# Kernel tuning notes

Measured on AMD Instinct MI355X. Metric: run time of the kernel, lower is better.

## Reference

```python
import jax, jax.numpy as jnp
import numpy as np

ANCHORS = np.array([116., 90., 156., 198., 373., 326.], np.float32).reshape(1, 1, 1, 3, 2)
IGNORE_THRESH = 0.5
OBJ_SCALE = 5.0
NOOBJ_SCALE = 1.0
XYWH_SCALE = 1.0
CLASS_SCALE = 1.0
GRID_SCALE = 1.0


def setup_inputs() -> dict:
    key = jax.random.key(0)
    k1, k2, k3 = jax.random.split(key, 3)
    B, GH, GW, NET, T, C = 16, 64, 64, 1024, 100, 80
    input_image = jnp.zeros((B, NET, NET, 3), jnp.float32)  # only shape is used
    y_pred = jax.random.normal(k1, (B, GH, GW, 3 * (5 + C)), jnp.float32)
    y_true = jax.random.uniform(k2, (B, GH, GW, 3, 5 + C), jnp.float32)
    true_boxes = jax.random.uniform(k3, (B, 1, 1, 1, T, 4), jnp.float32)
    return {"input_image": input_image, "y_pred": y_pred, "y_true": y_true, "true_boxes": true_boxes}


def reference(input_image, y_pred, y_true, true_boxes):
    B, GH, GW = y_true.shape[:3]
    net_h, net_w = input_image.shape[1], input_image.shape[2]
    dtype = y_pred.dtype
    anchors = jnp.asarray(ANCHORS, dtype)  # [1,1,1,3,2]
    y_pred = y_pred.reshape(B, GH, GW, 3, -1)
    object_mask = y_true[..., 4:5]  # [B,GH,GW,3,1]
    grid_factor = jnp.array([GW, GH], dtype).reshape(1, 1, 1, 1, 2)
    net_factor = jnp.array([net_w, net_h], dtype).reshape(1, 1, 1, 1, 2)
    cx, cy = jnp.meshgrid(jnp.arange(GW, dtype=dtype), jnp.arange(GH, dtype=dtype))
    cell_grid = jnp.stack([cx, cy], -1)[None, :, :, None, :]  # [1,GH,GW,1,2]

    # adjust predictions
    pred_box_xy = cell_grid + jax.nn.sigmoid(y_pred[..., :2])
    pred_box_wh = y_pred[..., 2:4]
    pred_box_conf = jax.nn.sigmoid(y_pred[..., 4:5])
    pred_box_class = y_pred[..., 5:]

    # adjust ground truth
    true_box_xy = y_true[..., 0:2]
    true_box_wh = y_true[..., 2:4]
    true_box_class = jnp.argmax(y_true[..., 5:], axis=-1)  # [B,GH,GW,3]

    # broadcast IoU: each predicted box vs all true boxes
    true_xy = true_boxes[..., 0:2] / grid_factor  # [B,1,1,1,T,2]
    true_wh = true_boxes[..., 2:4] / net_factor
    true_half = true_wh / 2.0
    true_mins, true_maxes = true_xy - true_half, true_xy + true_half
    pred_xy = (pred_box_xy / grid_factor)[..., None, :]  # [B,GH,GW,3,1,2]
    pred_wh = (jnp.exp(pred_box_wh) * anchors / net_factor)[..., None, :]
    pred_half = pred_wh / 2.0
    pred_mins, pred_maxes = pred_xy - pred_half, pred_xy + pred_half
    inter_wh = jnp.maximum(jnp.minimum(pred_maxes, true_maxes) - jnp.maximum(pred_mins, true_mins), 0.0)
    inter_area = inter_wh[..., 0] * inter_wh[..., 1]  # [B,GH,GW,3,T]
    true_area = true_wh[..., 0] * true_wh[..., 1]
    pred_area = pred_wh[..., 0] * pred_wh[..., 1]
    iou = inter_area / (pred_area + true_area - inter_area)
    best_ious = jnp.max(iou, axis=4)
    conf_ignore_mask = (best_ious > IGNORE_THRESH).astype(dtype)[..., None]

    # post-warmup branch (batch_seen > warmup_batches)
    xywh_mask = object_mask

    wh_scale = jnp.exp(true_box_wh) * anchors / net_factor
    wh_scale = (2.0 - wh_scale[..., 0] * wh_scale[..., 1])[..., None]

    xy_delta = xywh_mask * (true_box_xy - pred_box_xy) * wh_scale * XYWH_SCALE
    wh_delta = xywh_mask * (true_box_wh - pred_box_wh) * wh_scale * XYWH_SCALE
    conf_delta = (0.0 - pred_box_conf) * NOOBJ_SCALE
    conf_delta = conf_delta + object_mask * (1.0 - pred_box_conf) * OBJ_SCALE
    conf_delta = conf_delta * (1.0 - (1.0 - object_mask) * conf_ignore_mask)
    log_p = jax.nn.log_softmax(pred_box_class, axis=-1)
    ce = -jnp.take_along_axis(log_p, true_box_class[..., None], axis=-1)  # [B,GH,GW,3,1]
    class_delta = object_mask * ce * CLASS_SCALE

    delta = jnp.concatenate([xy_delta, wh_delta, conf_delta, class_delta], axis=-1)  # [B,GH,GW,3,6]
    loss = jnp.sum(jnp.square(delta), axis=(1, 2, 3, 4))
    return loss * GRID_SCALE
```

## Files before the change

kernel.cpp:

```cpp
#include <hip/hip_runtime.h>


#define NT 100
#define CPB 12288
#define NTOT 196608
#define ROWS_PER_BLOCK 64

typedef float f4 __attribute__((ext_vector_type(4)));
typedef f4 f4a __attribute__((aligned(4)));

__device__ __forceinline__ float frcp(float x) { return __builtin_amdgcn_rcpf(x); }
__device__ __forceinline__ float fsig(float x) { return frcp(1.f + __expf(-x)); }

__global__ __launch_bounds__(256) void yolo_loss_kernel(
    const float* __restrict__ y_pred,
    const float* __restrict__ y_true,
    const float* __restrict__ true_boxes,
    float* __restrict__ out)
{
    __shared__ f4 sbox[NT];
    __shared__ float swsum[4];

    const int tid = threadIdx.x;
    const int q   = tid & 3;
    const int row = blockIdx.x * ROWS_PER_BLOCK + (tid >> 2);
    const int b   = row / CPB;

    if (tid < NT) {
        const f4 tb = *(const f4*)(true_boxes + (size_t)b * NT * 4 + tid * 4);
        const float tx = tb.x * (1.f / 64.f),   ty = tb.y * (1.f / 64.f);
        const float tw = tb.z * (1.f / 1024.f), th = tb.w * (1.f / 1024.f);
        f4 r;
        r.x = tx - 0.5f * tw; r.y = ty - 0.5f * th;
        r.z = tx + 0.5f * tw; r.w = ty + 0.5f * th;
        sbox[tid] = r;
    }
    __syncthreads();

    const int rem = row % CPB;
    const int gy  = rem / 192;
    const int rr  = rem - gy * 192;
    const int gx  = rr / 3;
    const int a   = rr - gx * 3;
    const float aw = (a == 0) ? 116.f : ((a == 1) ? 156.f : 373.f);
    const float ah = (a == 0) ? 90.f  : ((a == 1) ? 198.f : 326.f);

    const float* p = y_pred + (size_t)row * 85;
    const float* t = y_true + (size_t)row * 85;

    const f4 g0 = *(const f4a*)p;
    const f4 g1 = *(const f4a*)(p + 4);
    const f4 h0 = *(const f4a*)t;
    const f4 h1 = *(const f4a*)(t + 4);

    const int ng = (q == 3) ? 4 : 5;
    f4 pg[5], tg[5];
#pragma unroll
    for (int k = 0; k < 5; ++k) {
        const int j  = 2 + q + 4 * k;
        const int jj = (j <= 20) ? j : 5;
        pg[k] = *(const f4a*)(p + 4 * jj);
        tg[k] = *(const f4a*)(t + 4 * jj);
    }
    float ptail = 0.f, ttail = 0.f;
    if (q == 3) { ptail = p[84]; ttail = t[84]; }

    const float p4v = g1.x, om = h1.x;

    float ssum = 0.f, tmax = -1e30f, psel = 0.f;
    int jm = 1 << 20;
    if (q == 0) {
#pragma unroll
        for (int e = 1; e < 4; ++e) {
            const float pv = g1[e], tv = h1[e];
            ssum += __expf(pv);
            const bool g = tv > tmax;
            tmax = g ? tv : tmax; psel = g ? pv : psel; jm = g ? (e - 1) : jm;
        }
    }
#pragma unroll
    for (int k = 0; k < 5; ++k) {
        if (k < ng) {
            const int j = 2 + q + 4 * k;
#pragma unroll
            for (int e = 0; e < 4; ++e) {
                const float pv = pg[k][e], tv = tg[k][e];
                ssum += __expf(pv);
                const bool g = tv > tmax;
                tmax = g ? tv : tmax; psel = g ? pv : psel;
                jm = g ? (4 * j + e - 5) : jm;
            }
        }
    }
    if (q == 3) {
        ssum += __expf(ptail);
        const bool g = ttail > tmax;
        tmax = g ? ttail : tmax; psel = g ? ptail : psel; jm = g ? 79 : jm;
    }
#pragma unroll
    for (int off = 1; off < 4; off <<= 1) {
        ssum += __shfl_xor(ssum, off, 64);
        const float otm = __shfl_xor(tmax, off, 64);
        const float ops = __shfl_xor(psel, off, 64);
        const int   ojm = __shfl_xor(jm, off, 64);
        const bool adopt = (otm > tmax) || (otm == tmax && ojm < jm);
        tmax = adopt ? otm : tmax; psel = adopt ? ops : psel; jm = adopt ? ojm : jm;
    }
    const float ce = __logf(ssum) - psel;

    const float predx = (float)gx + fsig(g0.x);
    const float predy = (float)gy + fsig(g0.y);
    const float conf  = fsig(p4v);
    const float pw  = __expf(g0.z) * aw * (1.f / 1024.f);
    const float phh = __expf(g0.w) * ah * (1.f / 1024.f);
    const float parea = pw * phh;
    const float px = predx * (1.f / 64.f), py = predy * (1.f / 64.f);
    const float pminx = px - 0.5f * pw,  pmaxx = px + 0.5f * pw;
    const float pminy = py - 0.5f * phh, pmaxy = py + 0.5f * phh;

    float best = 0.f;
#pragma unroll 5
    for (int k = 0; k < 25; ++k) {
        const f4 bx = sbox[q + 4 * k];
        float iw = fminf(pmaxx, bx.z) - fmaxf(pminx, bx.x);
        float ih = fminf(pmaxy, bx.w) - fmaxf(pminy, bx.y);
        iw = fmaxf(iw, 0.f); ih = fmaxf(ih, 0.f);
        const float inter = iw * ih;
        const float tarea = (bx.z - bx.x) * (bx.w - bx.y);
        best = fmaxf(best, inter * frcp(parea + tarea - inter));
    }
#pragma unroll
    for (int off = 1; off < 4; off <<= 1)
        best = fmaxf(best, __shfl_xor(best, off, 64));
    const float ignore = (best > 0.5f) ? 1.f : 0.f;

    const float wsx = __expf(h0.z) * aw * (1.f / 1024.f);
    const float wsy = __expf(h0.w) * ah * (1.f / 1024.f);
    const float ws  = 2.f - wsx * wsy;
    const float omws = om * ws;
    const float dx = omws * (h0.x - predx);
    const float dy = omws * (h0.y - predy);
    const float dw = omws * (h0.z - g0.z);
    const float dh = omws * (h0.w - g0.w);
    float dc = -conf + om * (1.f - conf) * 5.f;
    dc *= (1.f - (1.f - om) * ignore);
    const float dcl = om * ce;

    float val = dx * dx + dy * dy + dw * dw + dh * dh + dc * dc + dcl * dcl;
    val = (q == 0) ? val : 0.f;

#pragma unroll
    for (int off = 32; off > 0; off >>= 1) val += __shfl_down(val, off, 64);
    if ((tid & 63) == 0) swsum[tid >> 6] = val;
    __syncthreads();
    if (tid == 0) atomicAdd(out + b, swsum[0] + swsum[1] + swsum[2] + swsum[3]);
}

extern "C" void kernel_launch(void* const* d_in, const int* in_sizes, int n_in,
                              void* d_out, int out_size, void* d_ws, size_t ws_size,
                              hipStream_t stream) {
    const float* y_pred     = (const float*)d_in[1];
    const float* y_true     = (const float*)d_in[2];
    const float* true_boxes = (const float*)d_in[3];
    float* out = (float*)d_out;

    hipMemsetAsync(d_out, 0, (size_t)out_size * sizeof(float), stream);
    yolo_loss_kernel<<<NTOT / ROWS_PER_BLOCK, 256, 0, stream>>>(y_pred, y_true, true_boxes, out);
}
```

Measured before the change: 314.5 us.

## Stage rows through LDS with coalesced 16B loads and double-buffer two chunks

Each block now handles 128 rows in two 64-row chunks. Each chunk is loaded with fully coalesced 16-byte global loads into shared memory, replacing the per-thread unaligned row loads. The second chunk's global loads are issued before the first chunk is computed, so memory latency overlaps compute. In exchange the kernel uses about 44KB of LDS per block, which limits occupancy, and adds extra syncs and strided LDS reads that may hit bank conflicts.

```diff
diff --git a/kernel.cpp b/kernel.cpp
--- a/kernel.cpp
+++ b/kernel.cpp
@@ -4,10 +4,13 @@
 #define NT 100
 #define CPB 12288
 #define NTOT 196608
-#define ROWS_PER_BLOCK 64
+#define RPB 128
+#define CR 64
+#define ROW_DW 85
+#define CHUNK_DW (CR * ROW_DW)
+#define CHUNK_F4 (CHUNK_DW / 4)
 
 typedef float f4 __attribute__((ext_vector_type(4)));
-typedef f4 f4a __attribute__((aligned(4)));
 
 __device__ __forceinline__ float frcp(float x) { return __builtin_amdgcn_rcpf(x); }
 __device__ __forceinline__ float fsig(float x) { return frcp(1.f + __expf(-x)); }
@@ -18,13 +21,14 @@
     const float* __restrict__ true_boxes,
     float* __restrict__ out)
 {
+    __shared__ __align__(16) float sp[CHUNK_DW];
+    __shared__ __align__(16) float st[CHUNK_DW];
     __shared__ f4 sbox[NT];
     __shared__ float swsum[4];
 
     const int tid = threadIdx.x;
-    const int q   = tid & 3;
-    const int row = blockIdx.x * ROWS_PER_BLOCK + (tid >> 2);
-    const int b   = row / CPB;
+    const int block_row0 = blockIdx.x * RPB;
+    const int b = block_row0 / CPB;
 
     if (tid < NT) {
         const f4 tb = *(const f4*)(true_boxes + (size_t)b * NT * 4 + tid * 4);
@@ -35,123 +39,155 @@
         r.z = tx + 0.5f * tw; r.w = ty + 0.5f * th;
         sbox[tid] = r;
     }
-    __syncthreads();
-
-    const int rem = row % CPB;
-    const int gy  = rem / 192;
-    const int rr  = rem - gy * 192;
-    const int gx  = rr / 3;
-    const int a   = rr - gx * 3;
-    const float aw = (a == 0) ? 116.f : ((a == 1) ? 156.f : 373.f);
-    const float ah = (a == 0) ? 90.f  : ((a == 1) ? 198.f : 326.f);
-
-    const float* p = y_pred + (size_t)row * 85;
-    const float* t = y_true + (size_t)row * 85;
-
-    const f4 g0 = *(const f4a*)p;
-    const f4 g1 = *(const f4a*)(p + 4);
-    const f4 h0 = *(const f4a*)t;
-    const f4 h1 = *(const f4a*)(t + 4);
-
-    const int ng = (q == 3) ? 4 : 5;
-    f4 pg[5], tg[5];
-#pragma unroll
-    for (int k = 0; k < 5; ++k) {
-        const int j  = 2 + q + 4 * k;
-        const int jj = (j <= 20) ? j : 5;
-        pg[k] = *(const f4a*)(p + 4 * jj);
-        tg[k] = *(const f4a*)(t + 4 * jj);
-    }
-    float ptail = 0.f, ttail = 0.f;
-    if (q == 3) { ptail = p[84]; ttail = t[84]; }
-
-    const float p4v = g1.x, om = h1.x;
-
-    float ssum = 0.f, tmax = -1e30f, psel = 0.f;
-    int jm = 1 << 20;
-    if (q == 0) {
-#pragma unroll
-        for (int e = 1; e < 4; ++e) {
-            const float pv = g1[e], tv = h1[e];
-            ssum += __expf(pv);
-            const bool g = tv > tmax;
-            tmax = g ? tv : tmax; psel = g ? pv : psel; jm = g ? (e - 1) : jm;
-        }
-    }
-#pragma unroll
-    for (int k = 0; k < 5; ++k) {
-        if (k < ng) {
-            const int j = 2 + q + 4 * k;
+
+    const int R = tid >> 2;
+    const int q = tid & 3;
+
+    auto gload = [&](int c, f4* va, f4* wa) {
+        const size_t base = ((size_t)(block_row0 + c * CR) * ROW_DW) >> 2;
+        const f4* gp = (const f4*)y_pred + base;
+        const f4* gt = (const f4*)y_true + base;
+#pragma unroll
+        for (int i = 0; i < 6; ++i) {
+            const int idx = tid + 256 * i;
+            if (idx < CHUNK_F4) { va[i] = gp[idx]; wa[i] = gt[idx]; }
+        }
+    };
+    auto sstore = [&](const f4* va, const f4* wa) {
+        f4* dp = (f4*)sp; f4* dt = (f4*)st;
+#pragma unroll
+        for (int i = 0; i < 6; ++i) {
+            const int idx = tid + 256 * i;
+            if (idx < CHUNK_F4) { dp[idx] = va[i]; dt[idx] = wa[i]; }
+        }
+    };
+
+    auto consume = [&](int c) -> float {
+        const float* P = sp + R * ROW_DW;
+        const float* T = st + R * ROW_DW;
+
+        const int row = block_row0 + c * CR + R;
+        const int rem = row - b * CPB;
+        const int gy  = rem / 192;
+        const int rr  = rem - gy * 192;
+        const int gx  = rr / 3;
+        const int a   = rr - gx * 3;
+        const float aw = (a == 0) ? 116.f : ((a == 1) ? 156.f : 373.f);
+        const float ah = (a == 0) ? 90.f  : ((a == 1) ? 198.f : 326.f);
+
+        float hp[8], ht[8];
+#pragma unroll
+        for (int e = 0; e < 8; ++e) { hp[e] = P[e]; ht[e] = T[e]; }
+
+        float ssum = 0.f, tmax = -1e30f, psel = 0.f;
+        int jm = 1 << 20;
+        if (q == 0) {
+#pragma unroll
+            for (int e = 5; e < 8; ++e) {
+                const float pv = hp[e], tv = ht[e];
+                ssum += __expf(pv);
+                const bool g = tv > tmax;
+                tmax = g ? tv : tmax; psel = g ? pv : psel; jm = g ? (e - 5) : jm;
+            }
+        }
+#pragma unroll
+        for (int k = 0; k < 4; ++k) {
+            const int d0 = 8 + 4 * q + 16 * k;
 #pragma unroll
             for (int e = 0; e < 4; ++e) {
-                const float pv = pg[k][e], tv = tg[k][e];
+                const float pv = P[d0 + e], tv = T[d0 + e];
                 ssum += __expf(pv);
                 const bool g = tv > tmax;
                 tmax = g ? tv : tmax; psel = g ? pv : psel;
-                jm = g ? (4 * j + e - 5) : jm;
+                jm = g ? (d0 + e - 5) : jm;
             }
         }
-    }
-    if (q == 3) {
-        ssum += __expf(ptail);
-        const bool g = ttail > tmax;
-        tmax = g ? ttail : tmax; psel = g ? ptail : psel; jm = g ? 79 : jm;
-    }
-#pragma unroll
-    for (int off = 1; off < 4; off <<= 1) {
-        ssum += __shfl_xor(ssum, off, 64);
-        const float otm = __shfl_xor(tmax, off, 64);
-        const float ops = __shfl_xor(psel, off, 64);
-        const int   ojm = __shfl_xor(jm, off, 64);
-        const bool adopt = (otm > tmax) || (otm == tmax && ojm < jm);
-        tmax = adopt ? otm : tmax; psel = adopt ? ops : psel; jm = adopt ? ojm : jm;
-    }
-    const float ce = __logf(ssum) - psel;
-
-    const float predx = (float)gx + fsig(g0.x);
-    const float predy = (float)gy + fsig(g0.y);
-    const float conf  = fsig(p4v);
-    const float pw  = __expf(g0.z) * aw * (1.f / 1024.f);
-    const float phh = __expf(g0.w) * ah * (1.f / 1024.f);
-    const float parea = pw * phh;
-    const float px = predx * (1.f / 64.f), py = predy * (1.f / 64.f);
-    const float pminx = px - 0.5f * pw,  pmaxx = px + 0.5f * pw;
-    const float pminy = py - 0.5f * phh, pmaxy = py + 0.5f * phh;
-
-    float best = 0.f;
+        if (q < 3) {
+            const int d0 = 72 + 4 * q;
+#pragma unroll
+            for (int e = 0; e < 4; ++e) {
+                const float pv = P[d0 + e], tv = T[d0 + e];
+                ssum += __expf(pv);
+                const bool g = tv > tmax;
+                tmax = g ? tv : tmax; psel = g ? pv : psel;
+                jm = g ? (d0 + e - 5) : jm;
+            }
+        } else {
+            const float pv = P[84], tv = T[84];
+            ssum += __expf(pv);
+            const bool g = tv > tmax;
+            tmax = g ? tv : tmax; psel = g ? pv : psel; jm = g ? 79 : jm;
+        }
+#pragma unroll
+        for (int off = 1; off < 4; off <<= 1) {
+            ssum += __shfl_xor(ssum, off, 64);
+            const float otm = __shfl_xor(tmax, off, 64);
+            const float ops = __shfl_xor(psel, off, 64);
+            const int   ojm = __shfl_xor(jm, off, 64);
+            const bool adopt = (otm > tmax) || (otm == tmax && ojm < jm);
+            tmax = adopt ? otm : tmax; psel = adopt ? ops : psel; jm = adopt ? ojm : jm;
+        }
+        const float ce = __logf(ssum) - psel;
+
+        const float predx = (float)gx + fsig(hp[0]);
+        const float predy = (float)gy + fsig(hp[1]);
+        const float conf  = fsig(hp[4]);
+        const float pw  = __expf(hp[2]) * aw * (1.f / 1024.f);
+        const float phh = __expf(hp[3]) * ah * (1.f / 1024.f);
+        const float parea = pw * phh;
+        const float px = predx * (1.f / 64.f), py = predy * (1.f / 64.f);
+        const float pminx = px - 0.5f * pw,  pmaxx = px + 0.5f * pw;
+        const float pminy = py - 0.5f * phh, pmaxy = py + 0.5f * phh;
+
+        float best = 0.f;
 #pragma unroll 5
-    for (int k = 0; k < 25; ++k) {
-        const f4 bx = sbox[q + 4 * k];
-        float iw = fminf(pmaxx, bx.z) - fmaxf(pminx, bx.x);
-        float ih = fminf(pmaxy, bx.w) - fmaxf(pminy, bx.y);
-        iw = fmaxf(iw, 0.f); ih = fmaxf(ih, 0.f);
-        const float inter = iw * ih;
-        const float tarea = (bx.z - bx.x) * (bx.w - bx.y);
-        best = fmaxf(best, inter * frcp(parea + tarea - inter));
-    }
-#pragma unroll
-    for (int off = 1; off < 4; off <<= 1)
-        best = fmaxf(best, __shfl_xor(best, off, 64));
-    const float ignore = (best > 0.5f) ? 1.f : 0.f;
-
-    const float wsx = __expf(h0.z) * aw * (1.f / 1024.f);
-    const float wsy = __expf(h0.w) * ah * (1.f / 1024.f);
-    const float ws  = 2.f - wsx * wsy;
-    const float omws = om * ws;
-    const float dx = omws * (h0.x - predx);
-    const float dy = omws * (h0.y - predy);
-    const float dw = omws * (h0.z - g0.z);
-    const float dh = omws * (h0.w - g0.w);
-    float dc = -conf + om * (1.f - conf) * 5.f;
-    dc *= (1.f - (1.f - om) * ignore);
-    const float dcl = om * ce;
-
-    float val = dx * dx + dy * dy + dw * dw + dh * dh + dc * dc + dcl * dcl;
-    val = (q == 0) ? val : 0.f;
-
-#pragma unroll
-    for (int off = 32; off > 0; off >>= 1) val += __shfl_down(val, off, 64);
-    if ((tid & 63) == 0) swsum[tid >> 6] = val;
+        for (int k = 0; k < 25; ++k) {
+            const f4 bx = sbox[q + 4 * k];
+            float iw = fminf(pmaxx, bx.z) - fmaxf(pminx, bx.x);
+            float ih = fminf(pmaxy, bx.w) - fmaxf(pminy, bx.y);
+            iw = fmaxf(iw, 0.f); ih = fmaxf(ih, 0.f);
+            const float inter = iw * ih;
+            const float tarea = (bx.z - bx.x) * (bx.w - bx.y);
+            best = fmaxf(best, inter * frcp(parea + tarea - inter));
+        }
+#pragma unroll
+        for (int off = 1; off < 4; off <<= 1)
+            best = fmaxf(best, __shfl_xor(best, off, 64));
+        const float ignore = (best > 0.5f) ? 1.f : 0.f;
+
+        const float wsx = __expf(ht[2]) * aw * (1.f / 1024.f);
+        const float wsy = __expf(ht[3]) * ah * (1.f / 1024.f);
+        const float ws  = 2.f - wsx * wsy;
+        const float om  = ht[4];
+        const float omws = om * ws;
+        const float dx = omws * (ht[0] - predx);
+        const float dy = omws * (ht[1] - predy);
+        const float dw = omws * (ht[2] - hp[2]);
+        const float dh = omws * (ht[3] - hp[3]);
+        float dc = -conf + om * (1.f - conf) * 5.f;
+        dc *= (1.f - (1.f - om) * ignore);
+        const float dcl = om * ce;
+
+        const float val = dx * dx + dy * dy + dw * dw + dh * dh + dc * dc + dcl * dcl;
+        return (q == 0) ? val : 0.f;
+    };
+
+    f4 va[6], wa[6], vb[6], wb[6];
+    gload(0, va, wa);
+    sstore(va, wa);
+    __syncthreads();
+
+    gload(1, vb, wb);
+    float acc = consume(0);
+    __syncthreads();
+
+    sstore(vb, wb);
+    __syncthreads();
+    acc += consume(1);
+
+#pragma unroll
+    for (int off = 32; off > 0; off >>= 1) acc += __shfl_down(acc, off, 64);
+    if ((tid & 63) == 0) swsum[tid >> 6] = acc;
     __syncthreads();
     if (tid == 0) atomicAdd(out + b, swsum[0] + swsum[1] + swsum[2] + swsum[3]);
 }
@@ -165,5 +201,5 @@
     float* out = (float*)d_out;
 
     hipMemsetAsync(d_out, 0, (size_t)out_size * sizeof(float), stream);
-    yolo_loss_kernel<<<NTOT / ROWS_PER_BLOCK, 256, 0, stream>>>(y_pred, y_true, true_boxes, out);
+    yolo_loss_kernel<<<NTOT / RPB, 256, 0, stream>>>(y_pred, y_true, true_boxes, out);
 }
```

Result: slower. 326.1 us (+3.7%).
